# Kernel optimization log

Hardware: AMD Instinct MI355X
Metric: run time of the kernel (lower is better)

The kernel has to match this reference:

```python
import jax, jax.numpy as jnp
import numpy as np

N = 50000        # nodes
E = 800000       # edges (before self-loops)
IN_C = 256
OUT_C = 64
HEADS = 4
NEG_SLOPE = 0.2  # PyG GATConv default


def setup_inputs() -> dict:
    key = jax.random.key(0)
    k0, k1, k2, k3, k4 = jax.random.split(key, 5)
    x = jax.random.normal(k0, (N, IN_C), jnp.float32)
    edge_index = jax.random.randint(k1, (2, E), 0, N, dtype=jnp.int32)
    W = jax.random.normal(k2, (IN_C, HEADS * OUT_C), jnp.float32) * (1.0 / np.sqrt(IN_C))
    att_src = jax.random.normal(k3, (HEADS, OUT_C), jnp.float32) * 0.1
    att_dst = jax.random.normal(k4, (HEADS, OUT_C), jnp.float32) * 0.1
    bias = jnp.zeros((OUT_C,), jnp.float32)
    return {"x": x, "edge_index": edge_index, "W": W,
            "att_src": att_src, "att_dst": att_dst, "bias": bias}


def reference(x, edge_index, W, att_src, att_dst, bias):
    n = x.shape[0]
    # PyG GATConv default add_self_loops=True
    loop = jnp.arange(n, dtype=edge_index.dtype)
    src = jnp.concatenate([edge_index[0], loop])  # [E+N]
    dst = jnp.concatenate([edge_index[1], loop])  # [E+N]

    h = (x @ W).reshape(n, HEADS, OUT_C)                    # [N,H,C]
    a_src = jnp.einsum('nhc,hc->nh', h, att_src)            # [N,H]
    a_dst = jnp.einsum('nhc,hc->nh', h, att_dst)            # [N,H]

    e = jax.nn.leaky_relu(a_src[src] + a_dst[dst], NEG_SLOPE)   # [E',H]
    # segment softmax over edges grouped by destination node
    m = jax.lax.stop_gradient(jax.ops.segment_max(e, dst, num_segments=n))  # [N,H]
    ex = jnp.exp(e - m[dst])
    denom = jax.ops.segment_sum(ex, dst, num_segments=n)    # [N,H]
    alpha = ex / (denom[dst] + 1e-16)                       # [E',H]

    out = jax.ops.segment_sum(alpha[:, :, None] * h[src], dst, num_segments=n)  # [N,H,C]
    # concat=False -> mean over heads, then bias
    return out.mean(axis=1) + bias
```

## Files before the change

### kernel.cpp

```cpp
#include <hip/hip_runtime.h>
#include <hip/hip_bf16.h>

#define INC   256
#define HEADS 4
#define OUTC  64
#define NEG_SLOPE 0.2f
#define CAP   5120
#define EPB_A 4096

typedef __attribute__((ext_vector_type(8))) short  fragA;
typedef __attribute__((ext_vector_type(4))) float  f32x4;

__device__ __forceinline__ float bf2f(unsigned short u) {
    union { unsigned int i; float f; } v; v.i = ((unsigned int)u) << 16; return v.f;
}
__device__ __forceinline__ unsigned short f2bf(float x) {
    __hip_bfloat16 b = __float2bfloat16(x);
    return *reinterpret_cast<unsigned short*>(&b);
}

__global__ __launch_bounds__(256) void wt_zero_kernel(const float* __restrict__ W,
                                                      unsigned short* __restrict__ Wt,
                                                      int* __restrict__ btail, int nbuck)
{
    int idx = blockIdx.x * 256 + threadIdx.x;
    int k = idx >> 8, c = idx & 255;
    Wt[c * 256 + k] = f2bf(W[k * 256 + c]);
    if (idx < nbuck) btail[idx] = 0;
}

__global__ __launch_bounds__(256, 2) void gemm_passA(
    const float* __restrict__ A,
    const unsigned short* __restrict__ Wt,
    const float* __restrict__ att_src,
    const float* __restrict__ att_dst,
    unsigned short* __restrict__ H2,
    float* __restrict__ a_srcO,
    float* __restrict__ a_dstO,
    int M,
    const int* __restrict__ src, const int* __restrict__ dst,
    int* __restrict__ btail,
    int2* __restrict__ bucketbuf,
    int E, int nbA)
{
    __shared__ __align__(16) unsigned short As[64 * 256];
    const int tid = threadIdx.x;

    if ((int)blockIdx.x < nbA) {
        char* sm = (char*)As;
        int* lhist = (int*)sm;
        int* lrankc = (int*)(sm + 1024);
        int* gbase  = (int*)(sm + 2048);
        lhist[tid] = 0; lrankc[tid] = 0;
        __syncthreads();
        int e0 = blockIdx.x * EPB_A;
        int e1 = e0 + EPB_A; if (e1 > E) e1 = E;
        for (int e = e0 + tid; e < e1; e += 256)
            atomicAdd(&lhist[dst[e] >> 8], 1);
        __syncthreads();
        {
            int c = lhist[tid];
            gbase[tid] = (c > 0) ? atomicAdd(&btail[tid], c) : 0;
        }
        __syncthreads();
        for (int e = e0 + tid; e < e1; e += 256) {
            int s = src[e], d = dst[e];
            int b = d >> 8;
            int r = atomicAdd(&lrankc[b], 1);
            bucketbuf[(size_t)b * CAP + gbase[b] + r] = make_int2(s, d);
        }
        return;
    }

    const int lane = tid & 63;
    const int wave = tid >> 6;
    const int row0 = ((int)blockIdx.x - nbA) * 64;
    const int g   = lane >> 4;
    const int r16 = lane & 15;

    fragA b[4][8];
    {
        const unsigned short* wp = Wt + (size_t)(wave * 64) * 256;
        #pragma unroll
        for (int nn = 0; nn < 4; ++nn)
            #pragma unroll
            for (int kk = 0; kk < 8; ++kk)
                b[nn][kk] = *(const fragA*)(wp + (size_t)(nn * 16 + r16) * 256 + kk * 32 + g * 8);
    }

    #pragma unroll
    for (int i = 0; i < 16; ++i) {
        int f   = i * 256 + tid;
        int row = f >> 6;
        int q   = f & 63;
        int gr  = row0 + row;
        float4 v = (gr < M) ? *(const float4*)(A + (size_t)gr * INC + q * 4)
                            : make_float4(0.f, 0.f, 0.f, 0.f);
        ushort4 u;
        u.x = f2bf(v.x); u.y = f2bf(v.y); u.z = f2bf(v.z); u.w = f2bf(v.w);
        int byte = (row << 9) + (q << 3);
        byte ^= (row & 7) << 4;
        *(ushort4*)((char*)As + byte) = u;
    }
    __syncthreads();

    f32x4 acc[4][4] = {};
    #pragma unroll
    for (int kk = 0; kk < 8; ++kk) {
        fragA a[4];
        #pragma unroll
        for (int m = 0; m < 4; ++m) {
            int row  = m * 16 + r16;
            int byte = (row << 9) + ((kk * 32 + g * 8) << 1);
            byte ^= (row & 7) << 4;
            a[m] = *(const fragA*)((const char*)As + byte);
        }
        #pragma unroll
        for (int m = 0; m < 4; ++m)
            #pragma unroll
            for (int nn = 0; nn < 4; ++nn)
                acc[m][nn] = __builtin_amdgcn_mfma_f32_16x16x32_bf16(
                    a[m], b[nn][kk], acc[m][nn], 0, 0, 0);
    }

    #pragma unroll
    for (int m = 0; m < 4; ++m) {
        #pragma unroll
        for (int nn = 0; nn < 4; ++nn) {
            int gcol = wave * 64 + nn * 16 + r16;
            #pragma unroll
            for (int r = 0; r < 4; ++r) {
                int grow = row0 + m * 16 + g * 4 + r;
                if (grow < M)
                    H2[(size_t)grow * (HEADS * OUTC) + gcol] = f2bf(acc[m][nn][r]);
            }
        }
    }

    {
        float as_att[4], ad_att[4];
        #pragma unroll
        for (int nn = 0; nn < 4; ++nn) {
            as_att[nn] = att_src[wave * 64 + nn * 16 + r16];
            ad_att[nn] = att_dst[wave * 64 + nn * 16 + r16];
        }
        float sv[4][4], dv[4][4];
        #pragma unroll
        for (int m = 0; m < 4; ++m)
            #pragma unroll
            for (int r = 0; r < 4; ++r) {
                float s = 0.f, d = 0.f;
                #pragma unroll
                for (int nn = 0; nn < 4; ++nn) {
                    s = fmaf(acc[m][nn][r], as_att[nn], s);
                    d = fmaf(acc[m][nn][r], ad_att[nn], d);
                }
                sv[m][r] = s; dv[m][r] = d;
            }
        #pragma unroll
        for (int off = 1; off < 16; off <<= 1) {
            #pragma unroll
            for (int m = 0; m < 4; ++m)
                #pragma unroll
                for (int r = 0; r < 4; ++r) {
                    sv[m][r] += __shfl_xor(sv[m][r], off, 64);
                    dv[m][r] += __shfl_xor(dv[m][r], off, 64);
                }
        }
        #pragma unroll
        for (int m = 0; m < 4; ++m)
            #pragma unroll
            for (int r = 0; r < 4; ++r) {
                if (r16 == m * 4 + r) {
                    int grow = row0 + m * 16 + g * 4 + r;
                    if (grow < M) {
                        a_srcO[(size_t)grow * HEADS + wave] = sv[m][r];
                        a_dstO[(size_t)grow * HEADS + wave] = dv[m][r];
                    }
                }
            }
    }
}

__global__ __launch_bounds__(256) void passB_kernel(const int2* __restrict__ bucketbuf,
                                                    const int* __restrict__ btail,
                                                    int* __restrict__ offsets,
                                                    int2* __restrict__ esd,
                                                    int N, int E)
{
    __shared__ int lcnt[256];
    __shared__ int red[256];
    __shared__ unsigned short lrank[CAP];
    const int b = blockIdx.x, t = threadIdx.x;

    int s0 = 0;
    for (int j = t; j < b; j += 256) s0 += btail[j];
    red[t] = s0;
    __syncthreads();
    for (int off = 128; off > 0; off >>= 1) {
        if (t < off) red[t] += red[t + off];
        __syncthreads();
    }
    const int baseg = red[0];
    const int cnt = btail[b];
    __syncthreads();

    lcnt[t] = 0;
    __syncthreads();
    const int2* bb = bucketbuf + (size_t)b * CAP;
    for (int i = t; i < cnt; i += 256)
        lrank[i] = (unsigned short)atomicAdd(&lcnt[bb[i].y & 255], 1);
    __syncthreads();

    int v = lcnt[t];
    red[t] = v;
    __syncthreads();
    for (int off = 1; off < 256; off <<= 1) {
        int x = (t >= off) ? red[t - off] : 0;
        __syncthreads();
        red[t] += x;
        __syncthreads();
    }
    int excl = red[t] - v;
    lcnt[t] = excl;
    int node = b * 256 + t;
    if (node < N) offsets[node] = baseg + excl;
    if (b == 0 && t == 0) offsets[N] = E;
    __syncthreads();

    for (int i = t; i < cnt; i += 256) {
        int2 sd = bb[i];
        int slot = baseg + lcnt[sd.y & 255] + lrank[i];
        esd[slot] = sd;
    }
}

__global__ __launch_bounds__(256) void alpha2_kernel(const int2* __restrict__ esd,
                                                     const float* __restrict__ a_src,
                                                     const float* __restrict__ a_dst,
                                                     int* __restrict__ esrc,
                                                     float* __restrict__ palpha,
                                                     int E)
{
    int j = blockIdx.x * blockDim.x + threadIdx.x;
    if (j >= E) return;
    int2 sd = esd[j];
    float4 as = *(const float4*)(a_src + (size_t)sd.x * HEADS);
    float4 ad = *(const float4*)(a_dst + (size_t)sd.y * HEADS);
    float t, p0, p1, p2, p3;
    t = as.x + ad.x; t = t > 0.f ? t : NEG_SLOPE * t; p0 = __expf(t);
    t = as.y + ad.y; t = t > 0.f ? t : NEG_SLOPE * t; p1 = __expf(t);
    t = as.z + ad.z; t = t > 0.f ? t : NEG_SLOPE * t; p2 = __expf(t);
    t = as.w + ad.w; t = t > 0.f ? t : NEG_SLOPE * t; p3 = __expf(t);
    esrc[j] = sd.x;
    palpha[j]                   = p0;
    palpha[(size_t)E + j]       = p1;
    palpha[2 * (size_t)E + j]   = p2;
    palpha[3 * (size_t)E + j]   = p3;
}

__global__ __launch_bounds__(256) void fused_agg_kernel(
    const unsigned short* __restrict__ h2,
    const float* __restrict__ a_src,
    const float* __restrict__ a_dst,
    const int*   __restrict__ offsets,
    const int*   __restrict__ esrc,
    const float* __restrict__ palpha,
    const float* __restrict__ bias,
    float*       __restrict__ out,
    int n, int E)
{
    int i    = (int)((blockIdx.x * blockDim.x + threadIdx.x) >> 6);
    int lane = threadIdx.x & 63;
    if (i >= n) return;
    const int h  = lane >> 4;
    const int cg = lane & 15;

    float acc0, acc1, acc2, acc3, l;
    {
        float as = a_src[(size_t)i * HEADS + h];
        float ad = a_dst[(size_t)i * HEADS + h];
        float e = as + ad; e = e > 0.f ? e : NEG_SLOPE * e;
        float p = __expf(e);
        ushort4 v = *(const ushort4*)(h2 + (size_t)i * 256 + lane * 4);
        l = p;
        acc0 = p * bf2f(v.x);
        acc1 = p * bf2f(v.y);
        acc2 = p * bf2f(v.z);
        acc3 = p * bf2f(v.w);
    }

    const float* pa = palpha + (size_t)h * E;
    int beg = offsets[i], end = offsets[i + 1];
    int j = beg;
    for (; j + 3 < end; j += 4) {
        int s0 = esrc[j];
        int s1 = esrc[j + 1];
        int s2 = esrc[j + 2];
        int s3 = esrc[j + 3];
        float p0 = pa[j];
        float p1 = pa[j + 1];
        float p2 = pa[j + 2];
        float p3 = pa[j + 3];
        ushort4 v0 = *(const ushort4*)(h2 + (size_t)s0 * 256 + lane * 4);
        ushort4 v1 = *(const ushort4*)(h2 + (size_t)s1 * 256 + lane * 4);
        ushort4 v2 = *(const ushort4*)(h2 + (size_t)s2 * 256 + lane * 4);
        ushort4 v3 = *(const ushort4*)(h2 + (size_t)s3 * 256 + lane * 4);
        l += (p0 + p1) + (p2 + p3);
        acc0 = fmaf(p0, bf2f(v0.x), acc0);
        acc1 = fmaf(p0, bf2f(v0.y), acc1);
        acc2 = fmaf(p0, bf2f(v0.z), acc2);
        acc3 = fmaf(p0, bf2f(v0.w), acc3);
        acc0 = fmaf(p1, bf2f(v1.x), acc0);
        acc1 = fmaf(p1, bf2f(v1.y), acc1);
        acc2 = fmaf(p1, bf2f(v1.z), acc2);
        acc3 = fmaf(p1, bf2f(v1.w), acc3);
        acc0 = fmaf(p2, bf2f(v2.x), acc0);
        acc1 = fmaf(p2, bf2f(v2.y), acc1);
        acc2 = fmaf(p2, bf2f(v2.z), acc2);
        acc3 = fmaf(p2, bf2f(v2.w), acc3);
        acc0 = fmaf(p3, bf2f(v3.x), acc0);
        acc1 = fmaf(p3, bf2f(v3.y), acc1);
        acc2 = fmaf(p3, bf2f(v3.z), acc2);
        acc3 = fmaf(p3, bf2f(v3.w), acc3);
    }
    for (; j < end; ++j) {
        int s0 = esrc[j];
        float p0 = pa[j];
        ushort4 v0 = *(const ushort4*)(h2 + (size_t)s0 * 256 + lane * 4);
        l += p0;
        acc0 = fmaf(p0, bf2f(v0.x), acc0);
        acc1 = fmaf(p0, bf2f(v0.y), acc1);
        acc2 = fmaf(p0, bf2f(v0.z), acc2);
        acc3 = fmaf(p0, bf2f(v0.w), acc3);
    }

    float inv = 1.f / (l + 1e-16f);
    float r0 = acc0 * inv, r1 = acc1 * inv, r2 = acc2 * inv, r3 = acc3 * inv;

    r0 += __shfl_xor(r0, 16, 64); r0 += __shfl_xor(r0, 32, 64);
    r1 += __shfl_xor(r1, 16, 64); r1 += __shfl_xor(r1, 32, 64);
    r2 += __shfl_xor(r2, 16, 64); r2 += __shfl_xor(r2, 32, 64);
    r3 += __shfl_xor(r3, 16, 64); r3 += __shfl_xor(r3, 32, 64);

    if (lane < 16) {
        float4 b4 = *(const float4*)(bias + cg * 4);
        float4 o;
        o.x = 0.25f * r0 + b4.x;
        o.y = 0.25f * r1 + b4.y;
        o.z = 0.25f * r2 + b4.z;
        o.w = 0.25f * r3 + b4.w;
        *(float4*)(out + (size_t)i * OUTC + cg * 4) = o;
    }
}

extern "C" void kernel_launch(void* const* d_in, const int* in_sizes, int n_in,
                              void* d_out, int out_size, void* d_ws, size_t ws_size,
                              hipStream_t stream)
{
    (void)n_in; (void)out_size; (void)ws_size;
    const float* x       = (const float*)d_in[0];
    const int*   edge    = (const int*)d_in[1];
    const float* W       = (const float*)d_in[2];
    const float* att_src = (const float*)d_in[3];
    const float* att_dst = (const float*)d_in[4];
    const float* bias    = (const float*)d_in[5];
    float* out = (float*)d_out;

    const int N = in_sizes[0] / INC;
    const int E = in_sizes[1] / 2;
    const int* srcA = edge;
    const int* dstA = edge + E;
    const int nbuck = (N + 255) / 256;
    const int nbA   = (E + EPB_A - 1) / EPB_A;

    char* ws = (char*)d_ws;
    unsigned short* h2 = (unsigned short*)ws; ws += (size_t)N * (HEADS * OUTC) * sizeof(unsigned short);
    unsigned short* Wt = (unsigned short*)ws; ws += (size_t)256 * 256 * sizeof(unsigned short);
    float* a_src  = (float*)ws; ws += (size_t)N * HEADS * sizeof(float);
    float* a_dst  = (float*)ws; ws += (size_t)N * HEADS * sizeof(float);
    int* offsets  = (int*)ws;   ws += (size_t)(N + 1) * sizeof(int) + 12;
    int* btail    = (int*)ws;   ws += (size_t)256 * sizeof(int);
    int2* bucketbuf = (int2*)ws; ws += (size_t)nbuck * CAP * sizeof(int2);
    int2* esd     = (int2*)ws;  ws += (size_t)E * sizeof(int2);
    int* esrc     = (int*)ws;   ws += (size_t)E * sizeof(int);
    float* palpha = (float*)ws; ws += (size_t)4 * E * sizeof(float);

    wt_zero_kernel<<<256, 256, 0, stream>>>(W, Wt, btail, nbuck);

    gemm_passA<<<nbA + (N + 63) / 64, 256, 0, stream>>>(
        x, Wt, att_src, att_dst, h2, a_src, a_dst, N,
        srcA, dstA, btail, bucketbuf, E, nbA);

    passB_kernel<<<nbuck, 256, 0, stream>>>(bucketbuf, btail, offsets, esd, N, E);

    alpha2_kernel<<<(E + 255) / 256, 256, 0, stream>>>(esd, a_src, a_dst, esrc, palpha, E);

    fused_agg_kernel<<<(N + 3) / 4, 256, 0, stream>>>(h2, a_src, a_dst, offsets, esrc,
                                                      palpha, bias, out, N, E);
}
```

Before: 135.0 us.

## Fuse edge attention computation into aggregation kernel and drop alpha pass

Removes the separate alpha kernel and its esd/palpha buffers. passB now writes only the sorted source indices, and the aggregation kernel recomputes leaky-relu plus exp per edge from gathered a_src values. The edge loop is unrolled to 8 with vectorized int4 index loads after an alignment prologue. This saves one launch and the write and read of a 4xE float array, at the cost of recomputing exp in every lane and an extra scattered a_src gather per edge.

```diff
diff --git a/kernel.cpp b/kernel.cpp
--- a/kernel.cpp
+++ b/kernel.cpp
@@ -185,7 +185,7 @@
 __global__ __launch_bounds__(256) void passB_kernel(const int2* __restrict__ bucketbuf,
                                                     const int* __restrict__ btail,
                                                     int* __restrict__ offsets,
-                                                    int2* __restrict__ esd,
+                                                    int* __restrict__ esrc,
                                                     int N, int E)
 {
     __shared__ int lcnt[256];
@@ -231,32 +231,8 @@
     for (int i = t; i < cnt; i += 256) {
         int2 sd = bb[i];
         int slot = baseg + lcnt[sd.y & 255] + lrank[i];
-        esd[slot] = sd;
-    }
-}
-
-__global__ __launch_bounds__(256) void alpha2_kernel(const int2* __restrict__ esd,
-                                                     const float* __restrict__ a_src,
-                                                     const float* __restrict__ a_dst,
-                                                     int* __restrict__ esrc,
-                                                     float* __restrict__ palpha,
-                                                     int E)
-{
-    int j = blockIdx.x * blockDim.x + threadIdx.x;
-    if (j >= E) return;
-    int2 sd = esd[j];
-    float4 as = *(const float4*)(a_src + (size_t)sd.x * HEADS);
-    float4 ad = *(const float4*)(a_dst + (size_t)sd.y * HEADS);
-    float t, p0, p1, p2, p3;
-    t = as.x + ad.x; t = t > 0.f ? t : NEG_SLOPE * t; p0 = __expf(t);
-    t = as.y + ad.y; t = t > 0.f ? t : NEG_SLOPE * t; p1 = __expf(t);
-    t = as.z + ad.z; t = t > 0.f ? t : NEG_SLOPE * t; p2 = __expf(t);
-    t = as.w + ad.w; t = t > 0.f ? t : NEG_SLOPE * t; p3 = __expf(t);
-    esrc[j] = sd.x;
-    palpha[j]                   = p0;
-    palpha[(size_t)E + j]       = p1;
-    palpha[2 * (size_t)E + j]   = p2;
-    palpha[3 * (size_t)E + j]   = p3;
+        esrc[slot] = sd.x;
+    }
 }
 
 __global__ __launch_bounds__(256) void fused_agg_kernel(
@@ -265,10 +241,9 @@
     const float* __restrict__ a_dst,
     const int*   __restrict__ offsets,
     const int*   __restrict__ esrc,
-    const float* __restrict__ palpha,
     const float* __restrict__ bias,
     float*       __restrict__ out,
-    int n, int E)
+    int n)
 {
     int i    = (int)((blockIdx.x * blockDim.x + threadIdx.x) >> 6);
     int lane = threadIdx.x & 63;
@@ -276,10 +251,11 @@
     const int h  = lane >> 4;
     const int cg = lane & 15;
 
+    const float ad = a_dst[(size_t)i * HEADS + h];
+
     float acc0, acc1, acc2, acc3, l;
     {
         float as = a_src[(size_t)i * HEADS + h];
-        float ad = a_dst[(size_t)i * HEADS + h];
         float e = as + ad; e = e > 0.f ? e : NEG_SLOPE * e;
         float p = __expf(e);
         ushort4 v = *(const ushort4*)(h2 + (size_t)i * 256 + lane * 4);
@@ -290,23 +266,53 @@
         acc3 = p * bf2f(v.w);
     }
 
-    const float* pa = palpha + (size_t)h * E;
+#define EDGE_BODY(S, AS)                                                     \
+    {                                                                        \
+        float e_ = (AS) + ad; e_ = e_ > 0.f ? e_ : NEG_SLOPE * e_;           \
+        float p_ = __expf(e_);                                               \
+        ushort4 v_ = *(const ushort4*)(h2 + (size_t)(S) * 256 + lane * 4);   \
+        l += p_;                                                             \
+        acc0 = fmaf(p_, bf2f(v_.x), acc0);                                   \
+        acc1 = fmaf(p_, bf2f(v_.y), acc1);                                   \
+        acc2 = fmaf(p_, bf2f(v_.z), acc2);                                   \
+        acc3 = fmaf(p_, bf2f(v_.w), acc3);                                   \
+    }
+
     int beg = offsets[i], end = offsets[i + 1];
     int j = beg;
-    for (; j + 3 < end; j += 4) {
-        int s0 = esrc[j];
-        int s1 = esrc[j + 1];
-        int s2 = esrc[j + 2];
-        int s3 = esrc[j + 3];
-        float p0 = pa[j];
-        float p1 = pa[j + 1];
-        float p2 = pa[j + 2];
-        float p3 = pa[j + 3];
-        ushort4 v0 = *(const ushort4*)(h2 + (size_t)s0 * 256 + lane * 4);
-        ushort4 v1 = *(const ushort4*)(h2 + (size_t)s1 * 256 + lane * 4);
-        ushort4 v2 = *(const ushort4*)(h2 + (size_t)s2 * 256 + lane * 4);
-        ushort4 v3 = *(const ushort4*)(h2 + (size_t)s3 * 256 + lane * 4);
-        l += (p0 + p1) + (p2 + p3);
+    for (; j < end && (j & 3); ++j) {
+        int s = esrc[j];
+        float as = a_src[(size_t)s * HEADS + h];
+        EDGE_BODY(s, as);
+    }
+    for (; j + 7 < end; j += 8) {
+        int4 ea = *(const int4*)(esrc + j);
+        int4 eb = *(const int4*)(esrc + j + 4);
+        float as0 = a_src[(size_t)ea.x * HEADS + h];
+        float as1 = a_src[(size_t)ea.y * HEADS + h];
+        float as2 = a_src[(size_t)ea.z * HEADS + h];
+        float as3 = a_src[(size_t)ea.w * HEADS + h];
+        float as4 = a_src[(size_t)eb.x * HEADS + h];
+        float as5 = a_src[(size_t)eb.y * HEADS + h];
+        float as6 = a_src[(size_t)eb.z * HEADS + h];
+        float as7 = a_src[(size_t)eb.w * HEADS + h];
+        ushort4 v0 = *(const ushort4*)(h2 + (size_t)ea.x * 256 + lane * 4);
+        ushort4 v1 = *(const ushort4*)(h2 + (size_t)ea.y * 256 + lane * 4);
+        ushort4 v2 = *(const ushort4*)(h2 + (size_t)ea.z * 256 + lane * 4);
+        ushort4 v3 = *(const ushort4*)(h2 + (size_t)ea.w * 256 + lane * 4);
+        ushort4 v4 = *(const ushort4*)(h2 + (size_t)eb.x * 256 + lane * 4);
+        ushort4 v5 = *(const ushort4*)(h2 + (size_t)eb.y * 256 + lane * 4);
+        ushort4 v6 = *(const ushort4*)(h2 + (size_t)eb.z * 256 + lane * 4);
+        ushort4 v7 = *(const ushort4*)(h2 + (size_t)eb.w * 256 + lane * 4);
+        float e0 = as0 + ad; e0 = e0 > 0.f ? e0 : NEG_SLOPE * e0; float p0 = __expf(e0);
+        float e1 = as1 + ad; e1 = e1 > 0.f ? e1 : NEG_SLOPE * e1; float p1 = __expf(e1);
+        float e2 = as2 + ad; e2 = e2 > 0.f ? e2 : NEG_SLOPE * e2; float p2 = __expf(e2);
+        float e3 = as3 + ad; e3 = e3 > 0.f ? e3 : NEG_SLOPE * e3; float p3 = __expf(e3);
+        float e4 = as4 + ad; e4 = e4 > 0.f ? e4 : NEG_SLOPE * e4; float p4 = __expf(e4);
+        float e5 = as5 + ad; e5 = e5 > 0.f ? e5 : NEG_SLOPE * e5; float p5 = __expf(e5);
+        float e6 = as6 + ad; e6 = e6 > 0.f ? e6 : NEG_SLOPE * e6; float p6 = __expf(e6);
+        float e7 = as7 + ad; e7 = e7 > 0.f ? e7 : NEG_SLOPE * e7; float p7 = __expf(e7);
+        l += ((p0 + p1) + (p2 + p3)) + ((p4 + p5) + (p6 + p7));
         acc0 = fmaf(p0, bf2f(v0.x), acc0);
         acc1 = fmaf(p0, bf2f(v0.y), acc1);
         acc2 = fmaf(p0, bf2f(v0.z), acc2);
@@ -323,17 +329,41 @@
         acc1 = fmaf(p3, bf2f(v3.y), acc1);
         acc2 = fmaf(p3, bf2f(v3.z), acc2);
         acc3 = fmaf(p3, bf2f(v3.w), acc3);
+        acc0 = fmaf(p4, bf2f(v4.x), acc0);
+        acc1 = fmaf(p4, bf2f(v4.y), acc1);
+        acc2 = fmaf(p4, bf2f(v4.z), acc2);
+        acc3 = fmaf(p4, bf2f(v4.w), acc3);
+        acc0 = fmaf(p5, bf2f(v5.x), acc0);
+        acc1 = fmaf(p5, bf2f(v5.y), acc1);
+        acc2 = fmaf(p5, bf2f(v5.z), acc2);
+        acc3 = fmaf(p5, bf2f(v5.w), acc3);
+        acc0 = fmaf(p6, bf2f(v6.x), acc0);
+        acc1 = fmaf(p6, bf2f(v6.y), acc1);
+        acc2 = fmaf(p6, bf2f(v6.z), acc2);
+        acc3 = fmaf(p6, bf2f(v6.w), acc3);
+        acc0 = fmaf(p7, bf2f(v7.x), acc0);
+        acc1 = fmaf(p7, bf2f(v7.y), acc1);
+        acc2 = fmaf(p7, bf2f(v7.z), acc2);
+        acc3 = fmaf(p7, bf2f(v7.w), acc3);
+    }
+    if (j + 3 < end) {
+        int4 ea = *(const int4*)(esrc + j);
+        float as0 = a_src[(size_t)ea.x * HEADS + h];
+        float as1 = a_src[(size_t)ea.y * HEADS + h];
+        float as2 = a_src[(size_t)ea.z * HEADS + h];
+        float as3 = a_src[(size_t)ea.w * HEADS + h];
+        EDGE_BODY(ea.x, as0);
+        EDGE_BODY(ea.y, as1);
+        EDGE_BODY(ea.z, as2);
+        EDGE_BODY(ea.w, as3);
+        j += 4;
     }
     for (; j < end; ++j) {
-        int s0 = esrc[j];
-        float p0 = pa[j];
-        ushort4 v0 = *(const ushort4*)(h2 + (size_t)s0 * 256 + lane * 4);
-        l += p0;
-        acc0 = fmaf(p0, bf2f(v0.x), acc0);
-        acc1 = fmaf(p0, bf2f(v0.y), acc1);
-        acc2 = fmaf(p0, bf2f(v0.z), acc2);
-        acc3 = fmaf(p0, bf2f(v0.w), acc3);
-    }
+        int s = esrc[j];
+        float as = a_src[(size_t)s * HEADS + h];
+        EDGE_BODY(s, as);
+    }
+#undef EDGE_BODY
 
     float inv = 1.f / (l + 1e-16f);
     float r0 = acc0 * inv, r1 = acc1 * inv, r2 = acc2 * inv, r3 = acc3 * inv;
@@ -382,9 +412,7 @@
     int* offsets  = (int*)ws;   ws += (size_t)(N + 1) * sizeof(int) + 12;
     int* btail    = (int*)ws;   ws += (size_t)256 * sizeof(int);
     int2* bucketbuf = (int2*)ws; ws += (size_t)nbuck * CAP * sizeof(int2);
-    int2* esd     = (int2*)ws;  ws += (size_t)E * sizeof(int2);
     int* esrc     = (int*)ws;   ws += (size_t)E * sizeof(int);
-    float* palpha = (float*)ws; ws += (size_t)4 * E * sizeof(float);
 
     wt_zero_kernel<<<256, 256, 0, stream>>>(W, Wt, btail, nbuck);
 
@@ -392,10 +420,8 @@
         x, Wt, att_src, att_dst, h2, a_src, a_dst, N,
         srcA, dstA, btail, bucketbuf, E, nbA);
 
-    passB_kernel<<<nbuck, 256, 0, stream>>>(bucketbuf, btail, offsets, esd, N, E);
-
-    alpha2_kernel<<<(E + 255) / 256, 256, 0, stream>>>(esd, a_src, a_dst, esrc, palpha, E);
+    passB_kernel<<<nbuck, 256, 0, stream>>>(bucketbuf, btail, offsets, esrc, N, E);
 
     fused_agg_kernel<<<(N + 3) / 4, 256, 0, stream>>>(h2, a_src, a_dst, offsets, esrc,
-                                                      palpha, bias, out, N, E);
-}
+                                                      bias, out, N);
+}
```

New measurement: 129.1 us. 4.4% less time.
